# Optimization experiments

Measured on AMD Instinct MI355X. Metric: run time of the kernel, lower is better.

Reference implementation:

```python
import jax, jax.numpy as jnp
import numpy as np

N, D, C, T, E = 8192, 512, 4, 8, 32768
H = D  # hidden_nf == input_nf == output_nf (required by the module's own shapes)


def _silu(x):
    return x * jax.nn.sigmoid(x)


def _lin(x, W, b):
    # torch Linear convention: W is [out, in]
    y = jnp.einsum('...i,oi->...o', x, W)
    return y + b


def setup_inputs() -> dict:
    key = jax.random.key(0)
    ks = jax.random.split(key, 20)
    s = 0.05  # keep activations in a sane range through stacked SiLU MLPs
    return {
        'h': jax.random.normal(ks[0], (N, D), jnp.float32),
        'coord': jax.random.normal(ks[1], (N, C, 3), jnp.float32),
        'edge_attr': jax.random.normal(ks[2], (T, E, 1), jnp.float32),
        'edge_index': jax.random.randint(ks[3], (T, 2, E), 0, N),
        'mW1': jax.random.normal(ks[4], (H, 2 * D + C * C + 1), jnp.float32) * s,
        'mb1': jnp.zeros((H,), jnp.float32),
        'mW2': jax.random.normal(ks[5], (H, H), jnp.float32) * s,
        'mb2': jnp.zeros((H,), jnp.float32),
        'nW1': jax.random.normal(ks[6], (H, H + D), jnp.float32) * s,
        'nb1': jnp.zeros((H,), jnp.float32),
        'nW2': jax.random.normal(ks[7], (D, H), jnp.float32) * s,
        'nb2': jnp.zeros((D,), jnp.float32),
        'eW1': jax.random.normal(ks[8], (H, H + 1 + H), jnp.float32) * s,
        'eb1': jnp.zeros((H,), jnp.float32),
        'eW2': jax.random.normal(ks[9], (1, H), jnp.float32) * s,
        'eb2': jnp.zeros((1,), jnp.float32),
        'relW': jax.random.normal(ks[10], (T, D, H), jnp.float32) * s,
        'cW1': jax.random.normal(ks[11], (T, H, H), jnp.float32) * s,
        'cb1': jnp.zeros((T, H), jnp.float32),
        'cW2': jax.random.normal(ks[12], (T, C, H), jnp.float32) * (s * 0.001),  # xavier gain=0.001
    }


def reference(h, coord, edge_attr, edge_index, mW1, mb1, mW2, mb2,
              nW1, nb1, nW2, nb2, eW1, eb1, eW2, eb2, relW, cW1, cb1, cW2):
    n, d = h.shape
    t, _, e = edge_index.shape
    c = coord.shape[1]
    row = edge_index[:, 0]  # [T,E]
    col = edge_index[:, 1]

    # coord2radial (per type, vectorized over type axis)
    cd = coord[row] - coord[col]                              # [T,E,C,3]
    radial = jnp.einsum('teca,teda->tecd', cd, cd)            # [T,E,C,C]
    # F.normalize(radial, dim=0): L2-normalize across the edge axis of each type
    nrm = jnp.sqrt(jnp.sum(radial * radial, axis=1, keepdims=True))
    radial = radial / jnp.maximum(nrm, 1e-12)

    # message_model (dropout = identity in eval)
    feat = jnp.concatenate([h[row], h[col], radial.reshape(t, e, c * c), edge_attr], axis=-1)
    msg = _silu(_lin(_silu(_lin(feat, mW1, mb1)), mW2, mb2))  # [T,E,H]

    # node_model: per-type segment_sum -> per-type relation linear -> sum
    seg = jax.vmap(lambda dta, ids: jax.ops.segment_sum(dta, ids, num_segments=n))(msg, row)  # [T,N,H]
    agg = jnp.einsum('tnh,tdh->nd', seg, relW)                # sum over types
    h_new = h + _lin(_silu(_lin(jnp.concatenate([h, agg], axis=-1), nW1, nb1)), nW2, nb2)

    # coord_model: per-type coord MLP weights, segment-mean over all types' edges
    hid = _silu(jnp.einsum('teh,tgh->teg', msg, cW1) + cb1[:, None, :])
    w = jnp.einsum('teg,tcg->tec', hid, cW2)                  # [T,E,C]
    trans = cd * w[..., None]                                 # [T,E,C,3]
    rows_flat = row.reshape(-1)
    sumv = jax.ops.segment_sum(trans.reshape(t * e, c, 3), rows_flat, num_segments=n)
    cnt = jax.ops.segment_sum(jnp.ones((t * e,), trans.dtype), rows_flat, num_segments=n)
    x_new = coord + sumv / jnp.maximum(cnt, 1.0)[:, None, None]

    # edge_model (note: forward passes edge_attr here, not the messages)
    ef = jnp.concatenate([h_new[row], edge_attr, h_new[col]], axis=-1)  # [T,E,H+1+H]
    m = _lin(_silu(_lin(ef, eW1, eb1)), eW2, eb2)             # [T,E,1]

    return (h_new, x_new, m)
```

## Files before the change

### kernel.cpp

```cpp
#include <hip/hip_runtime.h>
#include <cstdint>

#define NN 8192
#define DD 512
#define CC 4
#define TT 8
#define EE 32768
#define TE (TT*EE)

typedef __attribute__((ext_vector_type(8))) short short8v;
typedef __attribute__((ext_vector_type(4))) float f32x4;
typedef unsigned int uint;

constexpr int FLAG_SILU = 1, FLAG_RES = 2, FLAG_WEPI = 4, FLAG_BIAS_T = 8;

__device__ __forceinline__ float silu_f(float x) {
  return x * __builtin_amdgcn_rcpf(1.f + __expf(-x));
}

__device__ __forceinline__ unsigned short f2bf(float f) {
  uint u = __builtin_bit_cast(uint, f);
  u += 0x7fffu + ((u >> 16) & 1u);
  return (unsigned short)(u >> 16);
}
__device__ __forceinline__ float bf2f(unsigned short b) {
  uint u = ((uint)b) << 16;
  return __builtin_bit_cast(float, u);
}
__device__ __forceinline__ float bflo(uint u) { return __builtin_bit_cast(float, u << 16); }
__device__ __forceinline__ float bfhi(uint u) { return __builtin_bit_cast(float, u & 0xffff0000u); }
__device__ __forceinline__ uint packbf(float a, float b) {
  return (uint)f2bf(a) | ((uint)f2bf(b) << 16);
}

__device__ __forceinline__ float wave_sum(float v) {
#pragma unroll
  for (int off = 32; off; off >>= 1) v += __shfl_xor(v, off);
  return v;
}

__device__ __forceinline__ void gload16(const void* g, void* l) {
  __builtin_amdgcn_global_load_lds(
      (const __attribute__((address_space(1))) void*)g,
      (__attribute__((address_space(3))) void*)l, 16, 0, 0);
}

__device__ __forceinline__ int xcd_swz(int i, int nwg) {
  return (i & 7) * (nwg >> 3) + (i >> 3);
}

struct AgDirect { const unsigned short* p; int K;
  __device__ const void* ptr(int m, int k, int) const { return p + (size_t)m * K + k; } };

struct AgHcat { const unsigned short* hb; const unsigned short* ab;
  __device__ const void* ptr(int m, int k, int) const {
    return (k < 512) ? (const void*)(hb + ((size_t)m << 9) + k)
                     : (const void*)(ab + ((size_t)m << 9) + (k - 512)); } };

struct AgSegG { const unsigned short* seg;
  __device__ const void* ptr(int m, int k, int) const {
    return seg + (((size_t)(k >> 9) * NN + m) << 9) + (k & 511); } };

struct BgDirect { const unsigned short* p; int K;
  __device__ const void* ptr(int o, int k, int) const { return p + (size_t)o * K + k; } };

struct BgRelG { const unsigned short* w;
  __device__ const void* ptr(int o, int k, int) const {
    return w + (((size_t)(k >> 9) * 512 + o) << 9) + (k & 511); } };

struct BgPerT { const unsigned short* w;
  __device__ const void* ptr(int o, int k, int tt) const {
    return w + (((size_t)tt << 18) + ((size_t)o << 9)) + k; } };

template<class AG, class BG>
__global__ __launch_bounds__(256)
void mgemm_k(AG ag, BG bg, int K, int tbase, int lognx,
             const float* __restrict__ bias, const float* __restrict__ res,
             float* __restrict__ outF, unsigned short* __restrict__ outB, int ldo, int flags)
{
  __shared__ __align__(16) unsigned short SM[128 * 136];
  unsigned short* As = SM;
  unsigned short* Bs = SM + 128 * 64;
  const int swz = xcd_swz(blockIdx.x, gridDim.x);
  const int xb = swz & ((1 << lognx) - 1), yb = swz >> lognx;
  const int m0 = yb * 128, o0 = xb * 128;
  const int tt = tbase + (m0 >> 15);
  const int tid = threadIdx.x, wave = tid >> 6, lane = tid & 63;
  const int wr = (wave >> 1) * 64, wc = (wave & 1) * 64;
  const int rs = lane >> 3, sl = lane & 7;

  f32x4 acc[4][4];
#pragma unroll
  for (int i = 0; i < 4; ++i)
#pragma unroll
    for (int j = 0; j < 4; ++j) acc[i][j] = (f32x4)0.f;

  for (int k0 = 0; k0 < K; k0 += 64) {
#pragma unroll
    for (int i = 0; i < 4; ++i) {
      int r = i * 32 + wave * 8 + rs;
      int slot = sl ^ (r & 7);
      gload16(ag.ptr(m0 + r, k0 + slot * 8, tt), &As[(i * 32 + wave * 8) * 64]);
    }
#pragma unroll
    for (int i = 0; i < 4; ++i) {
      int r = i * 32 + wave * 8 + rs;
      int slot = sl ^ (r & 7);
      gload16(bg.ptr(o0 + r, k0 + slot * 8, tt), &Bs[(i * 32 + wave * 8) * 64]);
    }
    __syncthreads();
    short8v a[4][2], b[4][2];
#pragma unroll
    for (int mi = 0; mi < 4; ++mi)
#pragma unroll
      for (int s = 0; s < 2; ++s) {
        int row = wr + mi * 16 + (lane & 15);
        int slot = (s * 4 + (lane >> 4)) ^ (row & 7);
        a[mi][s] = *(const short8v*)&As[row * 64 + slot * 8];
      }
#pragma unroll
    for (int ni = 0; ni < 4; ++ni)
#pragma unroll
      for (int s = 0; s < 2; ++s) {
        int row = wc + ni * 16 + (lane & 15);
        int slot = (s * 4 + (lane >> 4)) ^ (row & 7);
        b[ni][s] = *(const short8v*)&Bs[row * 64 + slot * 8];
      }
#pragma unroll
    for (int s = 0; s < 2; ++s)
#pragma unroll
      for (int mi = 0; mi < 4; ++mi)
#pragma unroll
        for (int ni = 0; ni < 4; ++ni)
          acc[mi][ni] = __builtin_amdgcn_mfma_f32_16x16x32_bf16(a[mi][s], b[ni][s], acc[mi][ni], 0, 0, 0);
    __syncthreads();
  }

  const int r4 = (lane >> 4) * 4, cl = lane & 15;
  if (outB && !outF) {
    unsigned short* Ep = SM;
#pragma unroll
    for (int mi = 0; mi < 4; ++mi)
#pragma unroll
      for (int ni = 0; ni < 4; ++ni)
#pragma unroll
        for (int rg = 0; rg < 4; ++rg) {
          int row = wr + mi * 16 + r4 + rg;
          int col = wc + ni * 16 + cl;
          float v = acc[mi][ni][rg];
          if (bias) v += (flags & FLAG_BIAS_T) ? bias[tt * 512 + o0 + col] : bias[o0 + col];
          if (flags & FLAG_SILU) v = silu_f(v);
          Ep[row * 136 + col] = f2bf(v);
        }
    __syncthreads();
#pragma unroll
    for (int p = 0; p < 8; ++p) {
      int idx = p * 256 + tid;
      int row = idx >> 4, ch = idx & 15;
      short8v vv = *(const short8v*)&Ep[row * 136 + ch * 8];
      *(short8v*)(outB + (size_t)(m0 + row) * ldo + o0 + ch * 8) = vv;
    }
    return;
  }
#pragma unroll
  for (int mi = 0; mi < 4; ++mi)
#pragma unroll
    for (int ni = 0; ni < 4; ++ni)
#pragma unroll
      for (int rg = 0; rg < 4; ++rg) {
        int row = m0 + wr + mi * 16 + r4 + rg;
        int col = o0 + wc + ni * 16 + cl;
        float v = acc[mi][ni][rg];
        if (bias) v += (flags & FLAG_BIAS_T) ? bias[tt * 512 + col] : bias[col];
        if (flags & FLAG_SILU) v = silu_f(v);
        if (flags & FLAG_RES) v += res[(size_t)row * ldo + col];
        if (outF) outF[(size_t)row * ldo + col] = v;
        if (outB) outB[(size_t)row * ldo + col] = f2bf(v);
      }
}

template<class AG, class BG>
__global__ __launch_bounds__(512)
void mgemm2_k(AG ag, BG bg, int K, int tbase,
              const float* __restrict__ bias,
              unsigned short* __restrict__ outB, int flags,
              const float* __restrict__ cw2, float* __restrict__ wpart, int wstride)
{
  __shared__ __align__(16) unsigned short SM[128 * 136];
  unsigned short* As = SM;
  unsigned short* Bs = SM + 128 * 64;
  const int swz = xcd_swz(blockIdx.x, gridDim.x);
  const int xb = swz & 3, yb = swz >> 2;
  const int m0 = yb * 128, o0 = xb * 128;
  const int tt = tbase + (m0 >> 15);
  const int tid = threadIdx.x, wave = tid >> 6, lane = tid & 63;
  const int wr = (wave >> 1) * 32, wc = (wave & 1) * 64;
  const int rs = lane >> 3, sl = lane & 7;

  f32x4 acc[2][4];
#pragma unroll
  for (int i = 0; i < 2; ++i)
#pragma unroll
    for (int j = 0; j < 4; ++j) acc[i][j] = (f32x4)0.f;

  for (int k0 = 0; k0 < K; k0 += 64) {
#pragma unroll
    for (int i = 0; i < 2; ++i) {
      int r = i * 64 + wave * 8 + rs;
      int slot = sl ^ (r & 7);
      gload16(ag.ptr(m0 + r, k0 + slot * 8, tt), &As[(i * 64 + wave * 8) * 64]);
    }
#pragma unroll
    for (int i = 0; i < 2; ++i) {
      int r = i * 64 + wave * 8 + rs;
      int slot = sl ^ (r & 7);
      gload16(bg.ptr(o0 + r, k0 + slot * 8, tt), &Bs[(i * 64 + wave * 8) * 64]);
    }
    __syncthreads();
    short8v a[2][2], b[4][2];
#pragma unroll
    for (int mi = 0; mi < 2; ++mi)
#pragma unroll
      for (int s = 0; s < 2; ++s) {
        int row = wr + mi * 16 + (lane & 15);
        int slot = (s * 4 + (lane >> 4)) ^ (row & 7);
        a[mi][s] = *(const short8v*)&As[row * 64 + slot * 8];
      }
#pragma unroll
    for (int ni = 0; ni < 4; ++ni)
#pragma unroll
      for (int s = 0; s < 2; ++s) {
        int row = wc + ni * 16 + (lane & 15);
        int slot = (s * 4 + (lane >> 4)) ^ (row & 7);
        b[ni][s] = *(const short8v*)&Bs[row * 64 + slot * 8];
      }
#pragma unroll
    for (int s = 0; s < 2; ++s)
#pragma unroll
      for (int mi = 0; mi < 2; ++mi)
#pragma unroll
        for (int ni = 0; ni < 4; ++ni)
          acc[mi][ni] = __builtin_amdgcn_mfma_f32_16x16x32_bf16(a[mi][s], b[ni][s], acc[mi][ni], 0, 0, 0);
    __syncthreads();
  }

  const int r4 = (lane >> 4) * 4, cl = lane & 15;
  if (flags & FLAG_WEPI) {
    const int slice = xb * 2 + (wave & 1);
    const float* cw2t = cw2 + tt * 2048;
    const float* bt = bias + tt * 512;
#pragma unroll
    for (int mi = 0; mi < 2; ++mi) {
      float sc[4][4];
#pragma unroll
      for (int rg = 0; rg < 4; ++rg)
#pragma unroll
        for (int c = 0; c < 4; ++c) sc[rg][c] = 0.f;
#pragma unroll
      for (int ni = 0; ni < 4; ++ni) {
        int col = o0 + wc + ni * 16 + cl;
        float c0 = cw2t[col], c1 = cw2t[512 + col], c2 = cw2t[1024 + col], c3 = cw2t[1536 + col];
        float bb = bt[col];
#pragma unroll
        for (int rg = 0; rg < 4; ++rg) {
          float v = silu_f(acc[mi][ni][rg] + bb);
          sc[rg][0] += v * c0; sc[rg][1] += v * c1; sc[rg][2] += v * c2; sc[rg][3] += v * c3;
        }
      }
#pragma unroll
      for (int rg = 0; rg < 4; ++rg)
#pragma unroll
        for (int c = 0; c < 4; ++c) {
          float s = sc[rg][c];
          s += __shfl_xor(s, 1); s += __shfl_xor(s, 2);
          s += __shfl_xor(s, 4); s += __shfl_xor(s, 8);
          sc[rg][c] = s;
        }
      int gp = m0 + wr + mi * 16 + r4 + (cl >> 2);
      wpart[(((size_t)slice * wstride) + gp) * 4 + (cl & 3)] = sc[cl >> 2][cl & 3];
    }
    return;
  }
  unsigned short* Ep = SM;
#pragma unroll
  for (int mi = 0; mi < 2; ++mi)
#pragma unroll
    for (int ni = 0; ni < 4; ++ni)
#pragma unroll
      for (int rg = 0; rg < 4; ++rg) {
        int row = wr + mi * 16 + r4 + rg;
        int col = wc + ni * 16 + cl;
        float v = acc[mi][ni][rg];
        v += bias[o0 + col];
        if (flags & FLAG_SILU) v = silu_f(v);
        Ep[row * 136 + col] = f2bf(v);
      }
  __syncthreads();
#pragma unroll
  for (int p = 0; p < 4; ++p) {
    int idx = p * 512 + tid;
    int row = idx >> 4, ch = idx & 15;
    short8v vv = *(const short8v*)&Ep[row * 136 + ch * 8];
    *(short8v*)(outB + (size_t)(m0 + row) * 512 + o0 + ch * 8) = vv;
  }
}

__global__ __launch_bounds__(256)
void prep_k(const float* h, const float* mW2, const float* nW1, const float* nW2,
            const float* relW, const float* cW1, const float* mW1, const float* eW1,
            const float* mb1, const float* eb1,
            unsigned short* hb, unsigned short* mW2b, unsigned short* nW1b,
            unsigned short* nW2b, unsigned short* relWb, unsigned short* cW1b,
            unsigned short* mW1pq, unsigned short* eGc, unsigned short* mW1t,
            float* wea, float* pqb, float* ggb)
{
  int i = blockIdx.x * 256 + threadIdx.x;
  if (i < 4194304) { hb[i] = f2bf(h[i]); return; }
  i -= 4194304;
  if (i < 262144) { mW2b[i] = f2bf(mW2[i]); return; }
  i -= 262144;
  if (i < 524288) { nW1b[i] = f2bf(nW1[i]); return; }
  i -= 524288;
  if (i < 262144) { nW2b[i] = f2bf(nW2[i]); return; }
  i -= 262144;
  if (i < 2097152) { relWb[i] = f2bf(relW[i]); return; }
  i -= 2097152;
  if (i < 2097152) { cW1b[i] = f2bf(cW1[i]); return; }
  i -= 2097152;
  if (i < 262144) { int r = i >> 9, k = i & 511; mW1pq[i] = f2bf(mW1[(size_t)r * 1041 + k]); return; }
  i -= 262144;
  if (i < 262144) { int r = i >> 9, k = i & 511; mW1pq[262144 + i] = f2bf(mW1[(size_t)r * 1041 + 512 + k]); return; }
  i -= 262144;
  if (i < 262144) { int r = i >> 9, k = i & 511; eGc[i] = f2bf(eW1[(size_t)r * 1025 + k]); return; }
  i -= 262144;
  if (i < 262144) { int r = i >> 9, k = i & 511; eGc[262144 + i] = f2bf(eW1[(size_t)r * 1025 + 513 + k]); return; }
  i -= 262144;
  if (i < 8704) { int j = i >> 9, c = i & 511; mW1t[i] = f2bf(mW1[(size_t)c * 1041 + 1024 + j]); return; }
  i -= 8704;
  if (i < 512) { wea[i] = eW1[(size_t)i * 1025 + 512]; return; }
  i -= 512;
  if (i < 1024) {
    pqb[i] = (i < 512) ? mb1[i] : 0.f;
    ggb[i] = (i < 512) ? eb1[i] : 0.f;
  }
}

__global__ __launch_bounds__(256)
void hist_k(const int* __restrict__ eidx, int* __restrict__ deg) {
  int id = blockIdx.x * 256 + threadIdx.x;
  int t = id >> 15, e = id & (EE - 1);
  atomicAdd(&deg[(t << 13) + eidx[(t << 16) + e]], 1);
}

__global__ __launch_bounds__(256)
void scan_k(const int* __restrict__ deg, int* __restrict__ off, int* __restrict__ cursor) {
  int t = blockIdx.x, tid = threadIdx.x;
  int base = (t << 13) + tid * 32;
  int loc[32]; int s = 0;
#pragma unroll
  for (int i = 0; i < 32; ++i) { loc[i] = deg[base + i]; s += loc[i]; }
  __shared__ int lds[256];
  lds[tid] = s;
  __syncthreads();
  for (int st = 1; st < 256; st <<= 1) {
    int x = (tid >= st) ? lds[tid - st] : 0;
    __syncthreads();
    lds[tid] += x;
    __syncthreads();
  }
  int run = lds[tid] - s;
#pragma unroll
  for (int i = 0; i < 32; ++i) {
    off[base + i] = run; cursor[base + i] = run; run += loc[i];
  }
}

__global__ __launch_bounds__(256)
void scatcd_k(const int* __restrict__ eidx, const float* __restrict__ ea,
              const float* __restrict__ coord, int* __restrict__ cursor,
              int* __restrict__ order, int* __restrict__ rowS, int* __restrict__ colS,
              float* __restrict__ eaS, float* __restrict__ cd,
              float* __restrict__ radial, float* __restrict__ pnrm)
{
  int m = blockIdx.x * 256 + threadIdx.x;
  int t = m >> 15, e = m & (EE - 1);
  int r = eidx[(t << 16) + e], c = eidx[(t << 16) + EE + e];
  int pos = atomicAdd(&cursor[(t << 13) + r], 1);
  size_t s = ((size_t)t << 15) + pos;
  order[s] = e; rowS[s] = r; colS[s] = c; eaS[s] = ea[m];
  const float4* cv4 = (const float4*)coord;
  float4 A0 = cv4[r * 3], A1 = cv4[r * 3 + 1], A2 = cv4[r * 3 + 2];
  float4 B0 = cv4[c * 3], B1 = cv4[c * 3 + 1], B2 = cv4[c * 3 + 2];
  float d[12] = {A0.x-B0.x, A0.y-B0.y, A0.z-B0.z, A0.w-B0.w,
                 A1.x-B1.x, A1.y-B1.y, A1.z-B1.z, A1.w-B1.w,
                 A2.x-B2.x, A2.y-B2.y, A2.z-B2.z, A2.w-B2.w};
  float4* cdv = (float4*)cd;
  cdv[s*3+0] = make_float4(d[0],d[1],d[2],d[3]);
  cdv[s*3+1] = make_float4(d[4],d[5],d[6],d[7]);
  cdv[s*3+2] = make_float4(d[8],d[9],d[10],d[11]);
  float rad[16], sq[16];
#pragma unroll
  for (int ci = 0; ci < 4; ++ci)
#pragma unroll
    for (int di = 0; di < 4; ++di) {
      float v = d[ci*3]*d[di*3] + d[ci*3+1]*d[di*3+1] + d[ci*3+2]*d[di*3+2];
      rad[ci*4+di] = v; sq[ci*4+di] = v * v;
    }
  float4* rv = (float4*)radial;
#pragma unroll
  for (int i = 0; i < 4; ++i)
    rv[s*4+i] = make_float4(rad[i*4], rad[i*4+1], rad[i*4+2], rad[i*4+3]);
#pragma unroll
  for (int i = 0; i < 16; ++i) sq[i] = wave_sum(sq[i]);
  __shared__ float red[4][16];
  int wv = threadIdx.x >> 6, lane = threadIdx.x & 63;
  if (lane == 0) {
#pragma unroll
    for (int i = 0; i < 16; ++i) red[wv][i] = sq[i];
  }
  __syncthreads();
  if (threadIdx.x < 16)
    pnrm[blockIdx.x * 16 + threadIdx.x] =
        red[0][threadIdx.x] + red[1][threadIdx.x] + red[2][threadIdx.x] + red[3][threadIdx.x];
}

__global__ __launch_bounds__(128)
void nrmred_k(const float* __restrict__ pnrm, float* __restrict__ nrm) {
  int t = threadIdx.x >> 4, j = threadIdx.x & 15;
  float s = 0.f;
  for (int b = 0; b < 128; ++b) s += pnrm[((t * 128 + b) << 4) + j];
  nrm[(t << 4) + j] = s;
}

__global__ __launch_bounds__(256)
void tails_k(const float* __restrict__ radial, const float* __restrict__ nrm,
             const float* __restrict__ eaS, unsigned short* __restrict__ tailm)
{
  int m = blockIdx.x * 256 + threadIdx.x;
  int t = m >> 15;
  unsigned short tmp[24];
#pragma unroll
  for (int j = 0; j < 16; ++j) {
    float r = radial[(size_t)m * 16 + j] / fmaxf(sqrtf(nrm[(t << 4) + j]), 1e-12f);
    tmp[j] = f2bf(r);
  }
  tmp[16] = f2bf(eaS[m]);
#pragma unroll
  for (int j = 17; j < 24; ++j) tmp[j] = 0;
  uint4* dst = (uint4*)(tailm + (size_t)m * 24);
  dst[0] = ((const uint4*)tmp)[0];
  dst[1] = ((const uint4*)tmp)[1];
  dst[2] = ((const uint4*)tmp)[2];
}

__global__ __launch_bounds__(256)
void msg1f_k(const unsigned short* __restrict__ PQ, const unsigned short* __restrict__ Wt,
             const unsigned short* __restrict__ tailm_g,
             const int* __restrict__ rowS_g, const int* __restrict__ colS_g,
             unsigned short* __restrict__ out)
{
  int tid = threadIdx.x;
  int e0 = xcd_swz(blockIdx.x, gridDim.x) * 8;
  uint wreg[17];
#pragma unroll
  for (int j = 0; j < 17; ++j) wreg[j] = *(const uint*)(Wt + j * 512 + tid * 2);
  for (int i = 0; i < 8; ++i) {
    int p = e0 + i;
    int r = rowS_g[p], c = colS_g[p];
    uint pv = *(const uint*)(PQ + ((size_t)r << 10) + tid * 2);
    uint qv = *(const uint*)(PQ + ((size_t)c << 10) + 512 + tid * 2);
    uint4 t0 = *(const uint4*)(tailm_g + (size_t)p * 24);
    uint4 t1 = *(const uint4*)(tailm_g + (size_t)p * 24 + 8);
    uint  t2 = *(const uint*)(tailm_g + (size_t)p * 24 + 16);
    float tl[17] = {bflo(t0.x), bfhi(t0.x), bflo(t0.y), bfhi(t0.y),
                    bflo(t0.z), bfhi(t0.z), bflo(t0.w), bfhi(t0.w),
                    bflo(t1.x), bfhi(t1.x), bflo(t1.y), bfhi(t1.y),
                    bflo(t1.z), bfhi(t1.z), bflo(t1.w), bfhi(t1.w),
                    bflo(t2)};
    float s0 = bflo(pv) + bflo(qv);
    float s1 = bfhi(pv) + bfhi(qv);
#pragma unroll
    for (int j = 0; j < 17; ++j) {
      s0 += tl[j] * bflo(wreg[j]); s1 += tl[j] * bfhi(wreg[j]);
    }
    *(uint*)(out + ((size_t)p << 9) + tid * 2) = packbf(silu_f(s0), silu_f(s1));
  }
}

__global__ __launch_bounds__(256)
void gsum_k(const unsigned short* __restrict__ msg, const int* __restrict__ offb,
            const int* __restrict__ deg, int tbase, unsigned short* __restrict__ segt)
{
  int l = xcd_swz(blockIdx.x, gridDim.x);
  int tloc = l >> 13, n = l & (NN - 1), tid = threadIdx.x;
  int t = tbase + tloc;
  int start = offb[(t << 13) + n], d = deg[(t << 13) + n];
  float s0 = 0.f, s1 = 0.f;
  const unsigned short* base = msg + (((size_t)tloc << 15) << 9);
  for (int j = 0; j < d; ++j) {
    uint v = *(const uint*)(base + ((size_t)(start + j) << 9) + tid * 2);
    s0 += bflo(v); s1 += bfhi(v);
  }
  *(uint*)(segt + (((size_t)tloc * NN + n) << 9) + tid * 2) = packbf(s0, s1);
}

__global__ __launch_bounds__(256)
void wsum_k(const float* __restrict__ wpart, float* __restrict__ wsum_out, int wstride) {
  int id = xcd_swz(blockIdx.x, gridDim.x) * 256 + threadIdx.x;
  float4 a = (float4){0.f, 0.f, 0.f, 0.f};
#pragma unroll
  for (int s = 0; s < 8; ++s) {
    float4 v = *(const float4*)&wpart[(((size_t)s * wstride) + id) * 4];
    a.x += v.x; a.y += v.y; a.z += v.z; a.w += v.w;
  }
  *(float4*)&wsum_out[(size_t)id * 4] = a;
}

__global__ __launch_bounds__(256)
void trxn_k(const float* __restrict__ coord, const float* __restrict__ cd,
            const float* __restrict__ wsum, const int* __restrict__ offb,
            const int* __restrict__ deg, float* __restrict__ xout)
{
  int id = blockIdx.x * 256 + threadIdx.x;
  int n = id / 12, j = id - n * 12, ci = j / 3;
  float s = 0.f; int cnt = 0;
#pragma unroll
  for (int t = 0; t < 8; ++t) {
    int o = offb[(t << 13) + n], d = deg[(t << 13) + n];
    size_t p = ((size_t)t << 15) + o;
    for (int k = 0; k < d; ++k)
      s += cd[(p + k) * 12 + j] * wsum[(p + k) * 4 + ci];
    cnt += d;
  }
  xout[id] = coord[id] + s / fmaxf((float)cnt, 1.f);
}

__global__ __launch_bounds__(256)
void mout_k(const unsigned short* __restrict__ GG,
            const float* __restrict__ eW2, const float* __restrict__ wea,
            const float* __restrict__ eb2, const float* __restrict__ eaS,
            const int* __restrict__ rowS, const int* __restrict__ colS,
            const int* __restrict__ order, float* __restrict__ out_m)
{
  int wbase = xcd_swz(blockIdx.x, gridDim.x) * 8 + (threadIdx.x >> 6) * 2;
  int lane = threadIdx.x & 63;
  int w0i = wbase, w1i = wbase + 1;
  int r0 = rowS[w0i], c0 = colS[w0i], r1 = rowS[w1i], c1 = colS[w1i];
  float ea0 = eaS[w0i], ea1 = eaS[w1i];
  short8v gv0  = *(const short8v*)(GG + ((size_t)r0 << 10) + lane * 8);
  short8v gcv0 = *(const short8v*)(GG + ((size_t)c0 << 10) + 512 + lane * 8);
  short8v gv1  = *(const short8v*)(GG + ((size_t)r1 << 10) + lane * 8);
  short8v gcv1 = *(const short8v*)(GG + ((size_t)c1 << 10) + 512 + lane * 8);
  const float4* w4 = (const float4*)(eW2 + lane * 8);
  const float4* a4 = (const float4*)(wea + lane * 8);
  float4 w0 = w4[0], w1 = w4[1], a0 = a4[0], a1 = a4[1];
  float wv8[8] = {w0.x,w0.y,w0.z,w0.w,w1.x,w1.y,w1.z,w1.w};
  float av8[8] = {a0.x,a0.y,a0.z,a0.w,a1.x,a1.y,a1.z,a1.w};
  float s0 = 0.f, s1 = 0.f;
#pragma unroll
  for (int j = 0; j < 8; ++j) {
    s0 += wv8[j] * silu_f(bf2f((unsigned short)gv0[j]) + bf2f((unsigned short)gcv0[j]) + ea0 * av8[j]);
    s1 += wv8[j] * silu_f(bf2f((unsigned short)gv1[j]) + bf2f((unsigned short)gcv1[j]) + ea1 * av8[j]);
  }
  s0 = wave_sum(s0);
  s1 = wave_sum(s1);
  if (lane == 0) {
    float eb = eb2[0];
    int t0 = w0i >> 15, t1 = w1i >> 15;
    out_m[((size_t)t0 << 15) + order[w0i]] = s0 + eb;
    out_m[((size_t)t1 << 15) + order[w1i]] = s1 + eb;
  }
}

extern "C" void kernel_launch(void* const* d_in, const int* in_sizes, int n_in,
                              void* d_out, int out_size, void* d_ws, size_t ws_size,
                              hipStream_t stream)
{
  const float* h     = (const float*)d_in[0];
  const float* coord = (const float*)d_in[1];
  const float* ea    = (const float*)d_in[2];
  const int*   eidx  = (const int*)  d_in[3];
  const float* mW1   = (const float*)d_in[4];
  const float* mb1   = (const float*)d_in[5];
  const float* mW2   = (const float*)d_in[6];
  const float* mb2   = (const float*)d_in[7];
  const float* nW1   = (const float*)d_in[8];
  const float* nb1   = (const float*)d_in[9];
  const float* nW2   = (const float*)d_in[10];
  const float* nb2   = (const float*)d_in[11];
  const float* eW1   = (const float*)d_in[12];
  const float* eb1   = (const float*)d_in[13];
  const float* eW2   = (const float*)d_in[14];
  const float* eb2   = (const float*)d_in[15];
  const float* relW  = (const float*)d_in[16];
  const float* cW1   = (const float*)d_in[17];
  const float* cb1   = (const float*)d_in[18];
  const float* cW2   = (const float*)d_in[19];

  float* out   = (float*)d_out;
  float* out_h = out;
  float* out_x = out + (size_t)NN * DD;
  float* out_m = out_x + (size_t)NN * CC * 3;

  char* ws = (char*)d_ws;
  size_t off = 0;
  auto alloc = [&](size_t bytes) -> void* {
    void* p = ws + off; off += (bytes + 255) & ~(size_t)255; return p;
  };
  float* cd     = (float*)alloc((size_t)TE * 12 * 4);
  unsigned short* tailm = (unsigned short*)alloc((size_t)TE * 24 * 2);
  float* agg    = (float*)alloc((size_t)NN * 512 * 4);
  unsigned short* h_bf  = (unsigned short*)alloc((size_t)NN * 512 * 2);
  unsigned short* hn_bf = (unsigned short*)alloc((size_t)NN * 512 * 2);
  unsigned short* PQb   = (unsigned short*)alloc((size_t)NN * 1024 * 2);
  unsigned short* GGb   = PQb;
  unsigned short* mW1pq = (unsigned short*)alloc((size_t)1024 * 512 * 2);
  unsigned short* mW1t  = (unsigned short*)alloc((size_t)17 * 512 * 2);
  unsigned short* mW2b  = (unsigned short*)alloc((size_t)512 * 512 * 2);
  unsigned short* nW1b  = (unsigned short*)alloc((size_t)512 * 1024 * 2);
  unsigned short* nW2b  = (unsigned short*)alloc((size_t)512 * 512 * 2);
  unsigned short* eGc   = (unsigned short*)alloc((size_t)1024 * 512 * 2);
  float* weab   = (float*)alloc(512 * 4);
  float* pqbias = (float*)alloc(1024 * 4);
  float* ggbias = (float*)alloc(1024 * 4);
  unsigned short* relWb = (unsigned short*)alloc((size_t)TT * 512 * 512 * 2);
  unsigned short* cW1b  = (unsigned short*)alloc((size_t)TT * 512 * 512 * 2);
  int* deg     = (int*)alloc((size_t)TT * NN * 4);
  int* offb    = (int*)alloc((size_t)TT * NN * 4);
  int* cursor  = (int*)alloc((size_t)TT * NN * 4);
  int* order   = (int*)alloc((size_t)TE * 4);
  int* rowS    = (int*)alloc((size_t)TE * 4);
  int* colS    = (int*)alloc((size_t)TE * 4);
  float* eaS   = (float*)alloc((size_t)TE * 4);
  float* wsumb = (float*)alloc((size_t)TE * 4 * 4);
  float* pnrm  = (float*)alloc((size_t)(TE / 256) * 16 * 4);
  float* nrm   = (float*)alloc((size_t)TT * 16 * 4);

  const size_t perG = (size_t)EE * 512 * 2 * 2 + (size_t)NN * 512 * 2 + (size_t)8 * EE * 16;
  int G = 4;
  while (G > 1 && off + (size_t)G * perG + (1 << 20) > ws_size) G >>= 1;
  unsigned short* bufA = (unsigned short*)alloc((size_t)G * EE * 512 * 2);
  unsigned short* bufB = (unsigned short*)alloc((size_t)G * EE * 512 * 2);
  unsigned short* segt = (unsigned short*)alloc((size_t)G * NN * 512 * 2);
  float* wpart = (float*)alloc((size_t)8 * G * EE * 4 * 4);
  unsigned short* aggb = segt;
  float* radial = (float*)bufA;

  hipMemsetAsync(deg, 0, (size_t)TT * NN * 4, stream);
  hipMemsetAsync(agg, 0, (size_t)NN * 512 * 4, stream);

  prep_k<<<41000, 256, 0, stream>>>(h, mW2, nW1, nW2, relW, cW1, mW1, eW1, mb1, eb1,
      h_bf, mW2b, nW1b, nW2b, relWb, cW1b, mW1pq, eGc, mW1t, weab, pqbias, ggbias);

  hist_k<<<TE / 256, 256, 0, stream>>>(eidx, deg);
  scan_k<<<TT, 256, 0, stream>>>(deg, offb, cursor);
  scatcd_k<<<TE / 256, 256, 0, stream>>>(eidx, ea, coord, cursor,
      order, rowS, colS, eaS, cd, radial, pnrm);
  nrmred_k<<<1, 128, 0, stream>>>(pnrm, nrm);
  tails_k<<<TE / 256, 256, 0, stream>>>(radial, nrm, eaS, tailm);

  mgemm_k<<<512, 256, 0, stream>>>(AgDirect{h_bf, 512}, BgDirect{mW1pq, 512}, 512, 0, 3,
      pqbias, nullptr, nullptr, PQb, 1024, 0);

  for (int g = 0; g < TT / G; ++g) {
    const int tbase = g * G;
    const size_t gb = (size_t)tbase << 15;
    msg1f_k<<<(G * EE) / 8, 256, 0, stream>>>(PQb, mW1t, tailm + gb * 24,
        rowS + gb, colS + gb, bufA);
    mgemm2_k<<<4 * (G * EE / 128), 512, 0, stream>>>(AgDirect{bufA, 512},
        BgDirect{mW2b, 512}, 512, tbase,
        mb2, bufB, FLAG_SILU, nullptr, nullptr, 0);
    gsum_k<<<G * NN, 256, 0, stream>>>(bufB, offb, deg, tbase, segt);
    bool last = (g == TT / G - 1);
    mgemm_k<<<4 * (NN / 128), 256, 0, stream>>>(AgSegG{segt},
        BgRelG{relWb + ((size_t)tbase << 18)}, G * 512, 0, 2,
        nullptr, agg, agg, last ? aggb : nullptr, 512, FLAG_RES);
    mgemm2_k<<<4 * (G * EE / 128), 512, 0, stream>>>(AgDirect{bufB, 512},
        BgPerT{cW1b}, 512, tbase,
        cb1, nullptr, FLAG_SILU | FLAG_WEPI | FLAG_BIAS_T, cW2, wpart, G * EE);
    wsum_k<<<(G * EE) / 256, 256, 0, stream>>>(wpart, wsumb + gb * 4, G * EE);
  }

  trxn_k<<<(NN * 12) / 256, 256, 0, stream>>>(coord, cd, wsumb, offb, deg, out_x);

  mgemm_k<<<4 * (NN / 128), 256, 0, stream>>>(AgHcat{h_bf, aggb}, BgDirect{nW1b, 1024}, 1024, 0, 2,
      nb1, nullptr, nullptr, bufA, 512, FLAG_SILU);
  mgemm_k<<<4 * (NN / 128), 256, 0, stream>>>(AgDirect{bufA, 512}, BgDirect{nW2b, 512}, 512, 0, 2,
      nb2, h, out_h, hn_bf, 512, FLAG_RES);

  mgemm_k<<<512, 256, 0, stream>>>(AgDirect{hn_bf, 512}, BgDirect{eGc, 512}, 512, 0, 3,
      ggbias, nullptr, nullptr, GGb, 1024, 0);
  mout_k<<<TE / 8, 256, 0, stream>>>(GGb, eW2, weab, eb2, eaS, rowS, colS, order, out_m);

  (void)in_sizes; (void)n_in; (void)out_size; (void)ws_size;
}
```

Baseline: 1.206 ms.

## Double-buffer LDS tiles in mgemm2 to overlap global loads with MFMA

The mgemm2 GEMM kernel now uses two LDS buffers and issues the global-to-LDS loads for the next K-slice before computing on the current one. It waits with an explicit vmcnt and raw s_barrier instead of __syncthreads. This is meant to hide global load latency behind the MFMA work. In exchange LDS use roughly doubles to 64KB per block, which may reduce occupancy, and the manual waitcnt counts must match the number of outstanding loads.

```diff
diff --git a/kernel.cpp b/kernel.cpp
--- a/kernel.cpp
+++ b/kernel.cpp
@@ -186,9 +186,7 @@
               unsigned short* __restrict__ outB, int flags,
               const float* __restrict__ cw2, float* __restrict__ wpart, int wstride)
 {
-  __shared__ __align__(16) unsigned short SM[128 * 136];
-  unsigned short* As = SM;
-  unsigned short* Bs = SM + 128 * 64;
+  __shared__ __align__(16) unsigned short SM[2][16384];
   const int swz = xcd_swz(blockIdx.x, gridDim.x);
   const int xb = swz & 3, yb = swz >> 2;
   const int m0 = yb * 128, o0 = xb * 128;
@@ -197,13 +195,12 @@
   const int wr = (wave >> 1) * 32, wc = (wave & 1) * 64;
   const int rs = lane >> 3, sl = lane & 7;
 
-  f32x4 acc[2][4];
-#pragma unroll
-  for (int i = 0; i < 2; ++i)
-#pragma unroll
-    for (int j = 0; j < 4; ++j) acc[i][j] = (f32x4)0.f;
-
-  for (int k0 = 0; k0 < K; k0 += 64) {
+  const int NK = K >> 6;
+
+  auto STAGE = [&](int bi, int ks) {
+    int k0 = ks * 64;
+    unsigned short* As = SM[bi];
+    unsigned short* Bs = SM[bi] + 128 * 64;
 #pragma unroll
     for (int i = 0; i < 2; ++i) {
       int r = i * 64 + wave * 8 + rs;
@@ -216,7 +213,27 @@
       int slot = sl ^ (r & 7);
       gload16(bg.ptr(o0 + r, k0 + slot * 8, tt), &Bs[(i * 64 + wave * 8) * 64]);
     }
-    __syncthreads();
+  };
+
+  f32x4 acc[2][4];
+#pragma unroll
+  for (int i = 0; i < 2; ++i)
+#pragma unroll
+    for (int j = 0; j < 4; ++j) acc[i][j] = (f32x4)0.f;
+
+  STAGE(0, 0);
+  for (int ks = 0; ks < NK; ++ks) {
+    int cur = ks & 1;
+    if (ks + 1 < NK) {
+      STAGE(cur ^ 1, ks + 1);
+      asm volatile("s_waitcnt vmcnt(4)" ::: "memory");
+    } else {
+      asm volatile("s_waitcnt vmcnt(0)" ::: "memory");
+    }
+    __builtin_amdgcn_s_barrier();
+    __builtin_amdgcn_sched_barrier(0);
+    const unsigned short* As = SM[cur];
+    const unsigned short* Bs = SM[cur] + 128 * 64;
     short8v a[2][2], b[4][2];
 #pragma unroll
     for (int mi = 0; mi < 2; ++mi)
@@ -241,7 +258,8 @@
 #pragma unroll
         for (int ni = 0; ni < 4; ++ni)
           acc[mi][ni] = __builtin_amdgcn_mfma_f32_16x16x32_bf16(a[mi][s], b[ni][s], acc[mi][ni], 0, 0, 0);
-    __syncthreads();
+    __builtin_amdgcn_sched_barrier(0);
+    __builtin_amdgcn_s_barrier();
   }
 
   const int r4 = (lane >> 4) * 4, cl = lane & 15;
@@ -281,7 +299,7 @@
     }
     return;
   }
-  unsigned short* Ep = SM;
+  unsigned short* Ep = SM[0];
 #pragma unroll
   for (int mi = 0; mi < 2; ++mi)
 #pragma unroll
```

Result: slower. 1.238 ms (+2.6%).
